# Kernel tuning notes

Measured on AMD Instinct MI355X. Metric: run time of the kernel, lower is better.

The kernel has to match this reference:

```python
import jax, jax.numpy as jnp
import numpy as np

D_MODEL = 1024
N_HEADS = 16
D_K = D_MODEL // N_HEADS
NEG = -1e9


def setup_inputs() -> dict:
    key = jax.random.key(0)
    ks = jax.random.split(key, 6)
    B, T, D = 4, 2048, D_MODEL
    s = 1.0 / np.sqrt(D)
    x = jax.random.normal(ks[0], (B, T, D), dtype=jnp.float32)
    Wq = jax.random.normal(ks[1], (D, D), dtype=jnp.float32) * s
    Wk = jax.random.normal(ks[2], (D, D), dtype=jnp.float32) * s
    Wv = jax.random.normal(ks[3], (D, D), dtype=jnp.float32) * s
    Wo = jax.random.normal(ks[4], (D, D), dtype=jnp.float32) * s
    bo = jnp.zeros((D,), dtype=jnp.float32)
    # causal mask: True above diagonal = masked (masked_fill where True)
    mask = jnp.triu(jnp.ones((T, T), dtype=bool), k=1)
    return {"x": x, "mask": mask, "Wq": Wq, "Wk": Wk, "Wv": Wv, "Wo": Wo, "bo": bo}


def reference(x, mask, Wq, Wk, Wv, Wo, bo):
    B, T, D = x.shape
    # torch nn.Linear: y = x @ W.T
    q = (x @ Wq.T).reshape(B, T, N_HEADS, D_K).transpose(0, 2, 1, 3)  # [B,H,T,dk]
    k = (x @ Wk.T).reshape(B, T, N_HEADS, D_K).transpose(0, 2, 1, 3)
    v = (x @ Wv.T).reshape(B, T, N_HEADS, D_K).transpose(0, 2, 1, 3)
    scores = jnp.einsum("bhqd,bhkd->bhqk", q, k) / np.sqrt(D_K)  # [B,H,T,T]
    scores = jnp.where(mask[:T, :T], NEG, scores)
    attn = jax.nn.softmax(scores, axis=-1)
    ctx = jnp.einsum("bhqk,bhkd->bhqd", attn, v)  # [B,H,T,dk]
    ctx = ctx.transpose(0, 2, 1, 3).reshape(B, T, D)
    return ctx @ Wo.T + bo
```

## Files before the change

kernel.cpp:

```cpp
#include <hip/hip_runtime.h>
#include <hip/hip_bf16.h>


typedef __attribute__((ext_vector_type(8))) short bf16x8;
typedef __attribute__((ext_vector_type(4))) float f32x4;

__device__ __forceinline__ unsigned short f2b(float x) {
  __hip_bfloat16 h = __float2bfloat16(x);
  return __builtin_bit_cast(unsigned short, h);
}

__device__ __forceinline__ void load_lds16(const void* g, void* l) {
  __builtin_amdgcn_global_load_lds((__attribute__((address_space(1))) void*)g,
                                   (__attribute__((address_space(3))) void*)l,
                                   16, 0, 0);
}

__global__ void cast_kernel(const float* __restrict__ x,
                            const float* __restrict__ w0, const float* __restrict__ w1,
                            const float* __restrict__ w2, const float* __restrict__ w3,
                            unsigned short* __restrict__ xb, unsigned short* __restrict__ wb) {
  int i = blockIdx.x * 256 + threadIdx.x;
  const float* src;
  unsigned short* dst;
  int c;
  if (i < 1048576) {
    src = x; dst = xb; c = i;
  } else {
    int cw = i - 1048576;
    int wi = cw >> 17;
    c = cw & 131071;
    src = (wi == 0) ? w0 : (wi == 1) ? w1 : (wi == 2) ? w2 : w3;
    dst = wb + ((size_t)wi << 20);
  }
  const float4* s4 = (const float4*)src;
  float4 a = s4[2 * c], b = s4[2 * c + 1];
  union { unsigned short u[8]; uint4 v; } r;
  r.u[0] = f2b(a.x); r.u[1] = f2b(a.y); r.u[2] = f2b(a.z); r.u[3] = f2b(a.w);
  r.u[4] = f2b(b.x); r.u[5] = f2b(b.y); r.u[6] = f2b(b.z); r.u[7] = f2b(b.w);
  ((uint4*)dst)[c] = r.v;
}

__launch_bounds__(256)
__global__ void gemm_qkv(const unsigned short* __restrict__ A,
                         const unsigned short* __restrict__ Bw,
                         unsigned short* __restrict__ Cout) {
  __shared__ unsigned short At[128 * 64];
  __shared__ unsigned short Bt[128 * 64];

  const int tid = threadIdx.x;
  const int lane = tid & 63;
  const int w = tid >> 6;
  const int quad = lane >> 4;
  const int l15 = lane & 15;
  const int m0 = blockIdx.x * 128;
  const int n0 = blockIdx.y * 128;
  const int wm = (w >> 1) * 64;
  const int wn = (w & 1) * 64;

  const f32x4 z4 = {0.f, 0.f, 0.f, 0.f};
  f32x4 acc[4][4];
#pragma unroll
  for (int i = 0; i < 4; ++i)
#pragma unroll
    for (int j = 0; j < 4; ++j) acc[i][j] = z4;

  for (int kt = 0; kt < 1024; kt += 64) {
    __syncthreads();
#pragma unroll
    for (int c = 0; c < 4; ++c) {
      int chunk = c * 256 + tid;
      int row = chunk >> 3;
      int scol = (chunk & 7) ^ (row & 7);
      load_lds16(A + (size_t)(m0 + row) * 1024 + kt + scol * 8,
                 &At[((c * 256 + (w << 6)) << 3)]);
      load_lds16(Bw + (size_t)(n0 + row) * 1024 + kt + scol * 8,
                 &Bt[((c * 256 + (w << 6)) << 3)]);
    }
    __syncthreads();
#pragma unroll
    for (int ks = 0; ks < 2; ++ks) {
      bf16x8 af[4], bf[4];
#pragma unroll
      for (int i = 0; i < 4; ++i) {
        int rowA = wm + i * 16 + l15;
        af[i] = *(const bf16x8*)&At[rowA * 64 + (((ks * 4 + quad) ^ (rowA & 7)) << 3)];
        int rowB = wn + i * 16 + l15;
        bf[i] = *(const bf16x8*)&Bt[rowB * 64 + (((ks * 4 + quad) ^ (rowB & 7)) << 3)];
      }
#pragma unroll
      for (int i = 0; i < 4; ++i)
#pragma unroll
        for (int j = 0; j < 4; ++j)
          acc[i][j] = __builtin_amdgcn_mfma_f32_16x16x32_bf16(af[i], bf[j], acc[i][j], 0, 0, 0);
    }
  }

  const int seg = n0 >> 10;
#pragma unroll
  for (int i = 0; i < 4; ++i) {
#pragma unroll
    for (int j = 0; j < 4; ++j) {
#pragma unroll
      for (int r = 0; r < 4; ++r) {
        int m = m0 + wm + i * 16 + quad * 4 + r;
        int n = n0 + wn + j * 16 + l15;
        int nn = n & 1023;
        float v = acc[i][j][r];
        if (seg == 0) {
          Cout[(size_t)m * 1024 + nn] = f2b(v);
        } else if (seg == 1) {
          (Cout + 8388608)[(size_t)m * 1024 + nn] = f2b(v);
        } else {
          int b = m >> 11, t = m & 2047, h = nn >> 6, d = nn & 63;
          (Cout + 16777216)[(((size_t)((b * 16 + h) * 64 + d)) << 11) + t] = f2b(v);
        }
      }
    }
  }
}

__launch_bounds__(256)
__global__ void gemm_proj(const unsigned short* __restrict__ A,
                          const unsigned short* __restrict__ Bw,
                          const float* __restrict__ bias,
                          float* __restrict__ out) {
  __shared__ unsigned short At[128 * 64];
  __shared__ unsigned short Bt[64 * 64];

  const int tid = threadIdx.x;
  const int lane = tid & 63;
  const int w = tid >> 6;
  const int quad = lane >> 4;
  const int l15 = lane & 15;
  const int m0 = blockIdx.x * 128;
  const int n0 = blockIdx.y * 64;
  const int wm = w * 32;

  const f32x4 z4 = {0.f, 0.f, 0.f, 0.f};
  f32x4 acc[2][4];
#pragma unroll
  for (int i = 0; i < 2; ++i)
#pragma unroll
    for (int j = 0; j < 4; ++j) acc[i][j] = z4;

  for (int kt = 0; kt < 1024; kt += 64) {
    __syncthreads();
#pragma unroll
    for (int c = 0; c < 4; ++c) {
      int chunk = c * 256 + tid;
      int row = chunk >> 3;
      int scol = (chunk & 7) ^ (row & 7);
      load_lds16(A + (size_t)(m0 + row) * 1024 + kt + scol * 8,
                 &At[((c * 256 + (w << 6)) << 3)]);
    }
#pragma unroll
    for (int c = 0; c < 2; ++c) {
      int chunk = c * 256 + tid;
      int row = chunk >> 3;
      int scol = (chunk & 7) ^ (row & 7);
      load_lds16(Bw + (size_t)(n0 + row) * 1024 + kt + scol * 8,
                 &Bt[((c * 256 + (w << 6)) << 3)]);
    }
    __syncthreads();
#pragma unroll
    for (int ks = 0; ks < 2; ++ks) {
      bf16x8 af[2], bf[4];
#pragma unroll
      for (int i = 0; i < 2; ++i) {
        int rowA = wm + i * 16 + l15;
        af[i] = *(const bf16x8*)&At[rowA * 64 + (((ks * 4 + quad) ^ (rowA & 7)) << 3)];
      }
#pragma unroll
      for (int j = 0; j < 4; ++j) {
        int rowB = j * 16 + l15;
        bf[j] = *(const bf16x8*)&Bt[rowB * 64 + (((ks * 4 + quad) ^ (rowB & 7)) << 3)];
      }
#pragma unroll
      for (int i = 0; i < 2; ++i)
#pragma unroll
        for (int j = 0; j < 4; ++j)
          acc[i][j] = __builtin_amdgcn_mfma_f32_16x16x32_bf16(af[i], bf[j], acc[i][j], 0, 0, 0);
    }
  }

#pragma unroll
  for (int i = 0; i < 2; ++i)
#pragma unroll
    for (int j = 0; j < 4; ++j) {
      int n = n0 + j * 16 + l15;
      float bv = bias[n];
#pragma unroll
      for (int r = 0; r < 4; ++r) {
        int m = m0 + wm + i * 16 + quad * 4 + r;
        out[(size_t)m * 1024 + n] = acc[i][j][r] + bv;
      }
    }
}

__launch_bounds__(256)
__global__ void attn_kernel(const unsigned short* __restrict__ Q,
                            const unsigned short* __restrict__ K,
                            const unsigned short* __restrict__ VT,
                            unsigned short* __restrict__ ctx) {
  __shared__ unsigned short Kt[2][64 * 64];
  __shared__ unsigned short Vt[2][64 * 64];
  __shared__ unsigned short Pt[64 * 64];

  const int tid = threadIdx.x;
  const int lane = tid & 63;
  const int w = tid >> 6;
  const int quad = lane >> 4;
  const int l15 = lane & 15;
  const int p = blockIdx.x;
  const int bh = blockIdx.y;
  const int b = bh >> 4, h = bh & 15;

  const unsigned short* Kg = K + ((size_t)(b * 2048)) * 1024 + h * 64;
  const unsigned short* Vg = VT + ((size_t)bh * 64) * 2048;

  const float SC = 0.1803368801f;
  const float M0 = 11.0f;

  for (int tt = 0; tt < 2; ++tt) {
    const int qt = tt ? (31 - p) : p;
    const int qb = qt * 64;

    const unsigned short* qbase =
        Q + ((size_t)(b * 2048 + qb + w * 16 + l15)) * 1024 + h * 64;
    bf16x8 qa[2];
    qa[0] = *(const bf16x8*)(qbase + quad * 8);
    qa[1] = *(const bf16x8*)(qbase + 32 + quad * 8);

    const f32x4 z4 = {0.f, 0.f, 0.f, 0.f};
    f32x4 o[4];
#pragma unroll
    for (int nt = 0; nt < 4; ++nt) o[nt] = z4;
    float lrow = 0.f;

    if (tt) __syncthreads();

#pragma unroll
    for (int c = 0; c < 2; ++c) {
      int chunk = c * 256 + tid;
      int row = chunk >> 3;
      int scol = (chunk & 7) ^ (row & 7);
      load_lds16(Kg + (size_t)row * 1024 + scol * 8, &Kt[0][((c * 256 + (w << 6)) << 3)]);
      load_lds16(Vg + ((size_t)row << 11) + scol * 8, &Vt[0][((c * 256 + (w << 6)) << 3)]);
    }

    int cur = 0;
    for (int j = 0; j <= qt; ++j) {
      const int j0 = j * 64;
      __syncthreads();

      if (j < qt) {
        const int nj0 = j0 + 64;
#pragma unroll
        for (int c = 0; c < 2; ++c) {
          int chunk = c * 256 + tid;
          int row = chunk >> 3;
          int scol = (chunk & 7) ^ (row & 7);
          load_lds16(Kg + (size_t)(nj0 + row) * 1024 + scol * 8,
                     &Kt[cur ^ 1][((c * 256 + (w << 6)) << 3)]);
          load_lds16(Vg + ((size_t)row << 11) + nj0 + scol * 8,
                     &Vt[cur ^ 1][((c * 256 + (w << 6)) << 3)]);
        }
      }

      f32x4 st[4];
#pragma unroll
      for (int nt = 0; nt < 4; ++nt) st[nt] = z4;
#pragma unroll
      for (int ks = 0; ks < 2; ++ks) {
#pragma unroll
        for (int nt = 0; nt < 4; ++nt) {
          int rowK = nt * 16 + l15;
          bf16x8 kf = *(const bf16x8*)&Kt[cur][rowK * 64 + (((ks * 4 + quad) ^ (rowK & 7)) << 3)];
          st[nt] = __builtin_amdgcn_mfma_f32_16x16x32_bf16(kf, qa[ks], st[nt], 0, 0, 0);
        }
      }

      const bool diag = (j == qt);
      const int q = qb + w * 16 + l15;
      float sum = 0.f;
#pragma unroll
      for (int nt = 0; nt < 4; ++nt) {
#pragma unroll
        for (int r = 0; r < 4; ++r) {
          float e = fmaf(st[nt][r], SC, -M0);
          if (diag) {
            int kpos = j0 + nt * 16 + quad * 4 + r;
            if (kpos > q) e = -1e30f;
          }
          float pv = exp2f(e);
          st[nt][r] = pv;
          sum += pv;
        }
      }
      sum += __shfl_xor(sum, 16);
      sum += __shfl_xor(sum, 32);
      lrow += sum;

      const int qrow = w * 16 + l15;
#pragma unroll
      for (int nt = 0; nt < 4; ++nt) {
        ushort4 pk;
        pk.x = f2b(st[nt][0]); pk.y = f2b(st[nt][1]);
        pk.z = f2b(st[nt][2]); pk.w = f2b(st[nt][3]);
        int chunk = nt * 4 + quad;
        *(ushort4*)&Pt[qrow * 64 + ((chunk ^ l15) << 2)] = pk;
      }

#pragma unroll
      for (int ks = 0; ks < 2; ++ks) {
        int c0 = ks * 8 + quad * 2;
        union { ushort4 hh[2]; bf16x8 v; } pu;
        pu.hh[0] = *(const ushort4*)&Pt[qrow * 64 + ((c0 ^ l15) << 2)];
        pu.hh[1] = *(const ushort4*)&Pt[qrow * 64 + (((c0 + 1) ^ l15) << 2)];
#pragma unroll
        for (int nt = 0; nt < 4; ++nt) {
          int rowV = nt * 16 + l15;
          bf16x8 vb = *(const bf16x8*)&Vt[cur][rowV * 64 + (((ks * 4 + quad) ^ (rowV & 7)) << 3)];
          o[nt] = __builtin_amdgcn_mfma_f32_16x16x32_bf16(pu.v, vb, o[nt], 0, 0, 0);
        }
      }
      cur ^= 1;
    }

    float lf[4];
#pragma unroll
    for (int r = 0; r < 4; ++r) lf[r] = 1.f / __shfl(lrow, quad * 4 + r);
#pragma unroll
    for (int nt = 0; nt < 4; ++nt) {
#pragma unroll
      for (int r = 0; r < 4; ++r) {
        int q = qb + w * 16 + quad * 4 + r;
        int dcol = nt * 16 + l15;
        ctx[((size_t)(b * 2048 + q)) * 1024 + h * 64 + dcol] = f2b(o[nt][r] * lf[r]);
      }
    }
  }
}

extern "C" void kernel_launch(void* const* d_in, const int* in_sizes, int n_in,
                              void* d_out, int out_size, void* d_ws, size_t ws_size,
                              hipStream_t stream) {
  const float* x  = (const float*)d_in[0];
  const float* Wq = (const float*)d_in[2];
  const float* Wk = (const float*)d_in[3];
  const float* Wv = (const float*)d_in[4];
  const float* Wo = (const float*)d_in[5];
  const float* bo = (const float*)d_in[6];
  float* out = (float*)d_out;

  unsigned short* xb  = (unsigned short*)d_ws;
  unsigned short* wb  = xb + 8388608;
  unsigned short* Qb  = wb + 4 * 1048576;
  unsigned short* Kb  = Qb + 8388608;
  unsigned short* VTb = Kb + 8388608;
  unsigned short* ctxb = xb;

  cast_kernel<<<6144, 256, 0, stream>>>(x, Wq, Wk, Wv, Wo, xb, wb);

  gemm_qkv<<<dim3(64, 24), 256, 0, stream>>>(xb, wb, Qb);

  attn_kernel<<<dim3(16, 64), 256, 0, stream>>>(Qb, Kb, VTb, ctxb);

  gemm_proj<<<dim3(64, 16), 256, 0, stream>>>(ctxb, wb + 3 * 1048576, bo, out);
}
```

Before: 301.8 us.

## Triple-buffer QKV GEMM with 256x128 tiles and interleaved async loads

The QKV projection GEMM now uses 512-thread blocks computing 256x128 tiles, with a three-stage LDS ring buffer fed by global_load_lds. Each k-step is split into two halves, and each half's loads for the tile two steps ahead are issued between its LDS reads and its MFMAs. Explicit vmcnt waits, barriers and setprio are meant to hide global-memory latency and raise MFMA utilisation. LDS use rises to about 144KB per block and grid size halves, which may limit occupancy and tail balance.

```diff
diff --git a/kernel.cpp b/kernel.cpp
--- a/kernel.cpp
+++ b/kernel.cpp
@@ -41,22 +41,37 @@
   ((uint4*)dst)[c] = r.v;
 }
 
-__launch_bounds__(256)
+__launch_bounds__(512, 2)
 __global__ void gemm_qkv(const unsigned short* __restrict__ A,
                          const unsigned short* __restrict__ Bw,
                          unsigned short* __restrict__ Cout) {
-  __shared__ unsigned short At[128 * 64];
-  __shared__ unsigned short Bt[128 * 64];
+  __shared__ unsigned short At[3][256 * 64];
+  __shared__ unsigned short Bt[3][128 * 64];
 
   const int tid = threadIdx.x;
   const int lane = tid & 63;
   const int w = tid >> 6;
   const int quad = lane >> 4;
   const int l15 = lane & 15;
-  const int m0 = blockIdx.x * 128;
+  const int m0 = blockIdx.x * 256;
   const int n0 = blockIdx.y * 128;
-  const int wm = (w >> 1) * 64;
-  const int wn = (w & 1) * 64;
+  const int wm = (w & 3) * 64;
+  const int wn = (w >> 2) * 64;
+
+  auto stageA = [&](int buf, int kt, int c) {
+    int chunk = c * 512 + tid;
+    int row = chunk >> 3;
+    int scol = (chunk & 7) ^ (row & 7);
+    load_lds16(A + (size_t)(m0 + row) * 1024 + kt + scol * 8,
+               &At[buf][(c * 512 + (w << 6)) << 3]);
+  };
+  auto stageB = [&](int buf, int kt, int c) {
+    int chunk = c * 512 + tid;
+    int row = chunk >> 3;
+    int scol = (chunk & 7) ^ (row & 7);
+    load_lds16(Bw + (size_t)(n0 + row) * 1024 + kt + scol * 8,
+               &Bt[buf][(c * 512 + (w << 6)) << 3]);
+  };
 
   const f32x4 z4 = {0.f, 0.f, 0.f, 0.f};
   f32x4 acc[4][4];
@@ -65,35 +80,87 @@
 #pragma unroll
     for (int j = 0; j < 4; ++j) acc[i][j] = z4;
 
-  for (int kt = 0; kt < 1024; kt += 64) {
-    __syncthreads();
-#pragma unroll
-    for (int c = 0; c < 4; ++c) {
-      int chunk = c * 256 + tid;
-      int row = chunk >> 3;
-      int scol = (chunk & 7) ^ (row & 7);
-      load_lds16(A + (size_t)(m0 + row) * 1024 + kt + scol * 8,
-                 &At[((c * 256 + (w << 6)) << 3)]);
-      load_lds16(Bw + (size_t)(n0 + row) * 1024 + kt + scol * 8,
-                 &Bt[((c * 256 + (w << 6)) << 3)]);
-    }
-    __syncthreads();
-#pragma unroll
-    for (int ks = 0; ks < 2; ++ks) {
-      bf16x8 af[4], bf[4];
-#pragma unroll
-      for (int i = 0; i < 4; ++i) {
-        int rowA = wm + i * 16 + l15;
-        af[i] = *(const bf16x8*)&At[rowA * 64 + (((ks * 4 + quad) ^ (rowA & 7)) << 3)];
-        int rowB = wn + i * 16 + l15;
-        bf[i] = *(const bf16x8*)&Bt[rowB * 64 + (((ks * 4 + quad) ^ (rowB & 7)) << 3)];
-      }
-#pragma unroll
-      for (int i = 0; i < 4; ++i)
-#pragma unroll
-        for (int j = 0; j < 4; ++j)
-          acc[i][j] = __builtin_amdgcn_mfma_f32_16x16x32_bf16(af[i], bf[j], acc[i][j], 0, 0, 0);
-    }
+#pragma unroll
+  for (int c = 0; c < 4; ++c) stageA(0, 0, c);
+#pragma unroll
+  for (int c = 0; c < 2; ++c) stageB(0, 0, c);
+#pragma unroll
+  for (int c = 0; c < 4; ++c) stageA(1, 64, c);
+#pragma unroll
+  for (int c = 0; c < 2; ++c) stageB(1, 64, c);
+  asm volatile("s_waitcnt vmcnt(6)" ::: "memory");
+  __builtin_amdgcn_s_barrier();
+  __builtin_amdgcn_sched_barrier(0);
+
+  int buf = 0;
+  for (int t = 0; t < 16; ++t) {
+    const int sbuf = (buf >= 1) ? buf - 1 : 2;
+    const int skt = (t + 2) * 64;
+    const bool st = (t < 14);
+
+    bf16x8 bfv[4][2];
+    bf16x8 afv[2][2];
+
+#pragma unroll
+    for (int j = 0; j < 4; ++j) {
+      int rowB = wn + j * 16 + l15;
+#pragma unroll
+      for (int ks = 0; ks < 2; ++ks)
+        bfv[j][ks] = *(const bf16x8*)&Bt[buf][rowB * 64 + (((ks * 4 + quad) ^ (rowB & 7)) << 3)];
+    }
+#pragma unroll
+    for (int ii = 0; ii < 2; ++ii) {
+      int rowA = wm + ii * 16 + l15;
+#pragma unroll
+      for (int ks = 0; ks < 2; ++ks)
+        afv[ii][ks] = *(const bf16x8*)&At[buf][rowA * 64 + (((ks * 4 + quad) ^ (rowA & 7)) << 3)];
+    }
+    if (st) { stageA(sbuf, skt, 0); stageA(sbuf, skt, 1); stageB(sbuf, skt, 0); }
+    __builtin_amdgcn_s_barrier();
+    __builtin_amdgcn_sched_barrier(0);
+    __builtin_amdgcn_s_setprio(1);
+#pragma unroll
+    for (int ii = 0; ii < 2; ++ii)
+#pragma unroll
+      for (int j = 0; j < 4; ++j)
+#pragma unroll
+        for (int ks = 0; ks < 2; ++ks)
+          acc[ii][j] = __builtin_amdgcn_mfma_f32_16x16x32_bf16(afv[ii][ks], bfv[j][ks],
+                                                               acc[ii][j], 0, 0, 0);
+    __builtin_amdgcn_s_setprio(0);
+    __builtin_amdgcn_s_barrier();
+    __builtin_amdgcn_sched_barrier(0);
+
+#pragma unroll
+    for (int ii = 0; ii < 2; ++ii) {
+      int rowA = wm + 32 + ii * 16 + l15;
+#pragma unroll
+      for (int ks = 0; ks < 2; ++ks)
+        afv[ii][ks] = *(const bf16x8*)&At[buf][rowA * 64 + (((ks * 4 + quad) ^ (rowA & 7)) << 3)];
+    }
+    if (st) { stageA(sbuf, skt, 2); stageA(sbuf, skt, 3); stageB(sbuf, skt, 1); }
+    __builtin_amdgcn_s_barrier();
+    __builtin_amdgcn_sched_barrier(0);
+    __builtin_amdgcn_s_setprio(1);
+#pragma unroll
+    for (int ii = 0; ii < 2; ++ii)
+#pragma unroll
+      for (int j = 0; j < 4; ++j)
+#pragma unroll
+        for (int ks = 0; ks < 2; ++ks)
+          acc[2 + ii][j] = __builtin_amdgcn_mfma_f32_16x16x32_bf16(afv[ii][ks], bfv[j][ks],
+                                                                   acc[2 + ii][j], 0, 0, 0);
+    __builtin_amdgcn_s_setprio(0);
+
+    if (t < 14) {
+      asm volatile("s_waitcnt vmcnt(6)" ::: "memory");
+    } else if (t == 14) {
+      asm volatile("s_waitcnt vmcnt(0)" ::: "memory");
+    }
+    __builtin_amdgcn_s_barrier();
+    __builtin_amdgcn_sched_barrier(0);
+
+    buf = (buf < 2) ? buf + 1 : 0;
   }
 
   const int seg = n0 >> 10;
@@ -112,8 +179,8 @@
         } else if (seg == 1) {
           (Cout + 8388608)[(size_t)m * 1024 + nn] = f2b(v);
         } else {
-          int b = m >> 11, t = m & 2047, h = nn >> 6, d = nn & 63;
-          (Cout + 16777216)[(((size_t)((b * 16 + h) * 64 + d)) << 11) + t] = f2b(v);
+          int b = m >> 11, tq = m & 2047, hh = nn >> 6, d = nn & 63;
+          (Cout + 16777216)[(((size_t)((b * 16 + hh) * 64 + d)) << 11) + tq] = f2b(v);
         }
       }
     }
@@ -363,7 +430,7 @@
 
   cast_kernel<<<6144, 256, 0, stream>>>(x, Wq, Wk, Wv, Wo, xb, wb);
 
-  gemm_qkv<<<dim3(64, 24), 256, 0, stream>>>(xb, wb, Qb);
+  gemm_qkv<<<dim3(32, 24), 512, 0, stream>>>(xb, wb, Qb);
 
   attn_kernel<<<dim3(16, 64), 256, 0, stream>>>(Qb, Kb, VTb, ctxb);
 
```

Measured after the change: 295.2 us. 2.2% less time.
